# Optimization experiments

Measured on AMD Instinct MI355X. Metric: run time of the kernel, lower is better.

The kernel has to match this reference:

```python
import jax, jax.numpy as jnp
import numpy as np

D_QKV = 64

def setup_inputs() -> dict:
    key = jax.random.key(0)
    k1, k2, k3, k4 = jax.random.split(key, 4)
    B, T, D = 4, 2048, 1024
    x = jax.random.normal(k1, (B, T, D), dtype=jnp.float32)
    Wq = jax.random.normal(k2, (D, D_QKV), dtype=jnp.float32) * (D ** -0.5)
    Wk = jax.random.normal(k3, (D, D_QKV), dtype=jnp.float32) * (D ** -0.5)
    Wv = jax.random.normal(k4, (D, D_QKV), dtype=jnp.float32) * (D ** -0.5)
    return {"x": x, "Wq": Wq, "Wk": Wk, "Wv": Wv}

def reference(x, Wq, Wk, Wv):
    # x: [B, T, D]; single-head causal attention with head dim d_qkv
    T = x.shape[1]
    q = jnp.einsum("btd,de->bte", x, Wq)  # [B, T, d]
    k = jnp.einsum("btd,de->bte", x, Wk)
    v = jnp.einsum("btd,de->bte", x, Wv)
    scores = jnp.einsum("bqe,bke->bqk", q, k) / (D_QKV ** 0.5)  # [B, T, T]
    causal = jnp.tril(jnp.ones((T, T), dtype=bool))
    scores = jnp.where(causal, scores, -jnp.inf)
    attn = jax.nn.softmax(scores, axis=2)
    return jnp.einsum("bqk,bke->bqe", attn, v)  # [B, T, d]
```

## Files before the change

kernel.cpp:

```cpp
#include <hip/hip_runtime.h>
#include <hip/hip_bf16.h>

typedef __hip_bfloat16 bf16;
typedef __bf16 bf16x8 __attribute__((ext_vector_type(8)));
typedef float f32x4 __attribute__((ext_vector_type(4)));
typedef unsigned short u16x8 __attribute__((ext_vector_type(8)));

#define B_SZ   4
#define T_SEQ  2048
#define D_IN   1024
#define D_QKV  64
#define BT     (B_SZ * T_SEQ)
#define PSTR   72

#define GLD_LDS(gp, lp) __builtin_amdgcn_global_load_lds(                     \
    (const __attribute__((address_space(1))) void*)(gp),                      \
    (__attribute__((address_space(3))) void*)(lp), 16, 0, 0)

__global__ __launch_bounds__(256) void wt_prep(
    const float* __restrict__ Wq, const float* __restrict__ Wk,
    const float* __restrict__ Wv, bf16* __restrict__ wt)
{
    __shared__ float ws[64 * 65];
    const int bx = blockIdx.x;
    const int m  = bx >> 4;
    const int k0 = (bx & 15) << 6;
    const float* W = (m == 0) ? Wq : (m == 1) ? Wk : Wv;
    const int tid = threadIdx.x;
    #pragma unroll
    for (int i = 0; i < 16; ++i) {
        const int idx = i * 256 + tid;
        const int kk = idx >> 6, nn = idx & 63;
        ws[kk * 65 + nn] = W[(size_t)(k0 + kk) * D_QKV + nn];
    }
    __syncthreads();
    const int n = tid >> 2, kq = (tid & 3) << 4;
    bf16 tmp[16];
    #pragma unroll
    for (int j = 0; j < 16; ++j)
        tmp[j] = __float2bfloat16(ws[(kq + j) * 65 + n]);
    uint4* dst = (uint4*)(wt + (size_t)(m * 64 + n) * D_IN + k0 + kq);
    dst[0] = ((uint4*)tmp)[0];
    dst[1] = ((uint4*)tmp)[1];
}

__global__ __launch_bounds__(256) void qkv_proj_mfma(
    const float* __restrict__ x, const bf16* __restrict__ wt,
    bf16* __restrict__ qb, bf16* __restrict__ kb, bf16* __restrict__ vt)
{
    __shared__ uint4 As[2][512];
    __shared__ uint4 Bs[2][768];

    const int tid  = threadIdx.x;
    const int wave = tid >> 6;
    const int lane = tid & 63;
    const int col  = lane & 15;
    const int quad = lane >> 4;
    const int bx   = blockIdx.x;
    const int m0   = (bx >> 1) * 32;
    const int ng   = bx & 1;

    f32x4 acc[3];
    #pragma unroll
    for (int i = 0; i < 3; ++i) acc[i] = (f32x4){0.f, 0.f, 0.f, 0.f};

    auto stage = [&](int it, int buf) {
        const int k0 = it * 64;
        #pragma unroll
        for (int j = 0; j < 5; ++j) {
            const int s = wave + j * 4;
            if (s < 8) {
                const int c = s * 64 + lane;
                const int r = c >> 4;
                const int ccl = ((c & 15) - r) & 15;
                const float* g = x + (size_t)(m0 + r) * D_IN + k0 + ccl * 4;
                GLD_LDS(g, &As[buf][s * 64]);
            } else {
                const int bs = s - 8;
                const int c = bs * 64 + lane;
                const int n = c >> 3;
                const int ccl = ((c & 7) - n) & 7;
                const bf16* g = wt + (size_t)(ng * 96 + n) * D_IN + k0 + ccl * 8;
                GLD_LDS(g, &Bs[buf][bs * 64]);
            }
        }
    };

    stage(0, 0);
    const int r  = (wave >> 1) * 16 + col;
    const int nh = wave & 1;
    #pragma unroll 1
    for (int it = 0; it < 16; ++it) {
        __syncthreads();
        if (it + 1 < 16) stage(it + 1, (it + 1) & 1);
        const float4* Ac = (const float4*)As[it & 1];
        const uint4*  Bc = Bs[it & 1];
        #pragma unroll
        for (int s = 0; s < 2; ++s) {
            const int ca = s * 8 + quad * 2;
            const float4 a0 = Ac[r * 16 + ((ca + r) & 15)];
            const float4 a1 = Ac[r * 16 + ((ca + 1 + r) & 15)];
            const bf16x8 af = (bf16x8){(__bf16)a0.x, (__bf16)a0.y, (__bf16)a0.z, (__bf16)a0.w,
                                       (__bf16)a1.x, (__bf16)a1.y, (__bf16)a1.z, (__bf16)a1.w};
            #pragma unroll
            for (int i = 0; i < 3; ++i) {
                const int n = nh * 48 + i * 16 + col;
                const bf16x8 bfr = __builtin_bit_cast(bf16x8,
                    Bc[n * 8 + ((s * 4 + quad + n) & 7)]);
                acc[i] = __builtin_amdgcn_mfma_f32_16x16x32_bf16(af, bfr, acc[i], 0, 0, 0);
            }
        }
    }

    const int bb = m0 >> 11;
    const int tl = m0 & (T_SEQ - 1);
    #pragma unroll
    for (int i = 0; i < 3; ++i) {
        const int n = ng * 96 + nh * 48 + i * 16 + col;
        #pragma unroll
        for (int rr = 0; rr < 4; ++rr) {
            const int row = m0 + (wave >> 1) * 16 + quad * 4 + rr;
            const bf16 vq = __float2bfloat16(acc[i][rr]);
            if (n < 64)       qb[(size_t)row * D_QKV + n] = vq;
            else if (n < 128) kb[(size_t)row * D_QKV + (n - 64)] = vq;
            else              vt[(size_t)bb * D_QKV * T_SEQ + (size_t)(n - 128) * T_SEQ
                                 + (tl + (wave >> 1) * 16 + quad * 4 + rr)] = vq;
        }
    }
}

__global__ __launch_bounds__(256) void attn_kernel(
    const bf16* __restrict__ qb, const bf16* __restrict__ kb,
    const bf16* __restrict__ vt, float* __restrict__ Op, float* __restrict__ lp)
{
    __shared__ uint4 Ks[2][512];
    __shared__ uint4 Vs[2][512];
    __shared__ unsigned short plds[4 * 16 * PSTR];

    const int tid  = threadIdx.x;
    const int wave = tid >> 6;
    const int lane = tid & 63;
    const int col  = lane & 15;
    const int quad = lane >> 4;
    const int bx   = blockIdx.x;
    const int tile    = (bx < 256) ? (127 - (bx >> 2)) : ((bx - 256) >> 2);
    const int quarter = bx & 3;
    const int b    = tile >> 5;
    const int qloc = (tile & 31) * 64;
    const int nch  = (tile & 31) + 1;

    const bf16* kbp = kb + (size_t)b * T_SEQ * D_QKV;
    const bf16* vtp = vt + (size_t)b * D_QKV * T_SEQ;
    const uint4* q4 = (const uint4*)(qb + (size_t)b * T_SEQ * D_QKV);

    const bf16x8 aq0 = __builtin_bit_cast(bf16x8, q4[(qloc + wave * 16 + col) * 8 + quad]);
    const bf16x8 aq1 = __builtin_bit_cast(bf16x8, q4[(qloc + wave * 16 + col) * 8 + 4 + quad]);

    f32x4 o[4];
    float ls[4];
    #pragma unroll
    for (int dt = 0; dt < 4; ++dt) o[dt] = (f32x4){0.f, 0.f, 0.f, 0.f};
    #pragma unroll
    for (int rr = 0; rr < 4; ++rr) ls[rr] = 0.f;

    unsigned short* pl = plds + wave * 16 * PSTR;
    const u16x8* p8 = (const u16x8*)pl;

    auto stage = [&](int c, int buf) {
        const int kb0 = c * 64;
        #pragma unroll
        for (int j = 0; j < 4; ++j) {
            const int s = wave + j * 4;
            if (s < 8) {
                const int ch = s * 64 + lane;
                const int key = ch >> 3;
                const int ccl = ((ch & 7) - key) & 7;
                const bf16* g = kbp + (size_t)(kb0 + key) * D_QKV + ccl * 8;
                GLD_LDS(g, &Ks[buf][s * 64]);
            } else {
                const int vs = s - 8;
                const int ch = vs * 64 + lane;
                const int d = ch >> 3;
                const int ccl = ((ch & 7) - d) & 7;
                const bf16* g = vtp + (size_t)d * T_SEQ + kb0 + ccl * 8;
                GLD_LDS(g, &Vs[buf][vs * 64]);
            }
        }
    };

    if (quarter < nch) stage(quarter, 0);
    int i = 0;
    for (int c = quarter; c < nch; c += 4, ++i) {
        __syncthreads();
        if (c + 4 < nch) stage(c + 4, (i + 1) & 1);
        const uint4* Kc = Ks[i & 1];
        const uint4* Vc = Vs[i & 1];

        f32x4 sc[4];
        #pragma unroll
        for (int nt = 0; nt < 4; ++nt) {
            const int kp = nt * 16 + col;
            const bf16x8 bk0 = __builtin_bit_cast(bf16x8, Kc[kp * 8 + ((quad + kp) & 7)]);
            const bf16x8 bk1 = __builtin_bit_cast(bf16x8, Kc[kp * 8 + ((4 + quad + kp) & 7)]);
            sc[nt] = (f32x4){0.f, 0.f, 0.f, 0.f};
            sc[nt] = __builtin_amdgcn_mfma_f32_16x16x32_bf16(aq0, bk0, sc[nt], 0, 0, 0);
            sc[nt] = __builtin_amdgcn_mfma_f32_16x16x32_bf16(aq1, bk1, sc[nt], 0, 0, 0);
        }

        if (c == nch - 1) {
            #pragma unroll
            for (int nt = 0; nt < 4; ++nt) {
                const int kp = c * 64 + nt * 16 + col;
                #pragma unroll
                for (int rr = 0; rr < 4; ++rr)
                    if (kp > qloc + wave * 16 + quad * 4 + rr) sc[nt][rr] = -INFINITY;
            }
        }

        #pragma unroll
        for (int nt = 0; nt < 4; ++nt) {
            #pragma unroll
            for (int rr = 0; rr < 4; ++rr) {
                const float pv = __expf(sc[nt][rr] * 0.125f);
                ls[rr] += pv;
                pl[(quad * 4 + rr) * PSTR + nt * 16 + col] =
                    __builtin_bit_cast(unsigned short, __float2bfloat16(pv));
            }
        }

        const bf16x8 pa0 = __builtin_bit_cast(bf16x8, p8[col * 9 + quad]);
        const bf16x8 pa1 = __builtin_bit_cast(bf16x8, p8[col * 9 + 4 + quad]);

        #pragma unroll
        for (int dt = 0; dt < 4; ++dt) {
            const int dp = dt * 16 + col;
            const bf16x8 bv0 = __builtin_bit_cast(bf16x8, Vc[dp * 8 + ((quad + dp) & 7)]);
            const bf16x8 bv1 = __builtin_bit_cast(bf16x8, Vc[dp * 8 + ((4 + quad + dp) & 7)]);
            o[dt] = __builtin_amdgcn_mfma_f32_16x16x32_bf16(pa0, bv0, o[dt], 0, 0, 0);
            o[dt] = __builtin_amdgcn_mfma_f32_16x16x32_bf16(pa1, bv1, o[dt], 0, 0, 0);
        }
    }

    #pragma unroll
    for (int rr = 0; rr < 4; ++rr) {
        #pragma unroll
        for (int msk = 1; msk < 16; msk <<= 1)
            ls[rr] += __shfl_xor(ls[rr], msk);
    }

    const int pbase = (tile * 4 + quarter) * 64 + wave * 16;
    #pragma unroll
    for (int dt = 0; dt < 4; ++dt)
        #pragma unroll
        for (int rr = 0; rr < 4; ++rr)
            Op[(size_t)(pbase + quad * 4 + rr) * D_QKV + dt * 16 + col] = o[dt][rr];
    if (col == 0) {
        #pragma unroll
        for (int rr = 0; rr < 4; ++rr)
            lp[pbase + quad * 4 + rr] = ls[rr];
    }
}

__global__ __launch_bounds__(256) void combine_attn(
    const float* __restrict__ Op, const float* __restrict__ lp,
    float* __restrict__ out)
{
    const int idx = blockIdx.x * 256 + threadIdx.x;
    const int qg = idx >> 6, d = idx & 63;
    const int tile = qg >> 6, qq = qg & 63;
    float s = 0.f, l = 0.f;
    #pragma unroll
    for (int k = 0; k < 4; ++k) {
        s += Op[(size_t)((tile * 4 + k) * 64 + qq) * D_QKV + d];
        l += lp[(tile * 4 + k) * 64 + qq];
    }
    out[(size_t)qg * D_QKV + d] = s / l;
}

extern "C" void kernel_launch(void* const* d_in, const int* in_sizes, int n_in,
                              void* d_out, int out_size, void* d_ws, size_t ws_size,
                              hipStream_t stream) {
    const float* x  = (const float*)d_in[0];
    const float* Wq = (const float*)d_in[1];
    const float* Wk = (const float*)d_in[2];
    const float* Wv = (const float*)d_in[3];
    float* out = (float*)d_out;

    char* ws = (char*)d_ws;
    bf16*  qb = (bf16*)(ws);
    bf16*  kb = (bf16*)(ws + (1u << 20));
    bf16*  vt = (bf16*)(ws + (2u << 20));
    bf16*  wt = (bf16*)(ws + (3u << 20));
    float* Op = (float*)(ws + (4u << 20));
    float* lp = (float*)(ws + (12u << 20));

    wt_prep<<<48, 256, 0, stream>>>(Wq, Wk, Wv, wt);
    qkv_proj_mfma<<<512, 256, 0, stream>>>(x, wt, qb, kb, vt);
    attn_kernel<<<512, 256, 0, stream>>>(qb, kb, vt, Op, lp);
    combine_attn<<<2048, 256, 0, stream>>>(Op, lp, out);
}
```

Before: 109.5 us.

## Stream-K balance causal attention work and widen QKV projection tiles

The attention kernel now flattens all 2112 causal (query tile, key chunk) items and hands each of the 512 blocks an equal contiguous slice. A block carries its running accumulators across chunks of the same query tile and writes a partial result whenever a tile ends or its slice ends. The combine kernel walks each tile's chunks and sums only the partials written by distinct owning blocks. Separately, the QKV projection block now computes 16 rows against all 192 output columns, so x is read once instead of twice. The cost is a larger partial-output workspace (lp moved to 40MB) and a serial combine loop per query.

```diff
diff --git a/kernel.cpp b/kernel.cpp
--- a/kernel.cpp
+++ b/kernel.cpp
@@ -1,5 +1,6 @@
 #include <hip/hip_runtime.h>
 #include <hip/hip_bf16.h>
+#include <math.h>
 
 typedef __hip_bfloat16 bf16;
 typedef __bf16 bf16x8 __attribute__((ext_vector_type(8)));
@@ -12,6 +13,8 @@
 #define D_QKV  64
 #define BT     (B_SZ * T_SEQ)
 #define PSTR   72
+#define TOTW   2112
+#define ANB    512
 
 #define GLD_LDS(gp, lp) __builtin_amdgcn_global_load_lds(                     \
     (const __attribute__((address_space(1))) void*)(gp),                      \
@@ -48,17 +51,15 @@
     const float* __restrict__ x, const bf16* __restrict__ wt,
     bf16* __restrict__ qb, bf16* __restrict__ kb, bf16* __restrict__ vt)
 {
-    __shared__ uint4 As[2][512];
-    __shared__ uint4 Bs[2][768];
+    __shared__ uint4 As[2][256];
+    __shared__ uint4 Bs[2][1536];
 
     const int tid  = threadIdx.x;
     const int wave = tid >> 6;
     const int lane = tid & 63;
     const int col  = lane & 15;
     const int quad = lane >> 4;
-    const int bx   = blockIdx.x;
-    const int m0   = (bx >> 1) * 32;
-    const int ng   = bx & 1;
+    const int m0   = blockIdx.x * 16;
 
     f32x4 acc[3];
     #pragma unroll
@@ -67,28 +68,27 @@
     auto stage = [&](int it, int buf) {
         const int k0 = it * 64;
         #pragma unroll
-        for (int j = 0; j < 5; ++j) {
+        for (int j = 0; j < 7; ++j) {
             const int s = wave + j * 4;
-            if (s < 8) {
+            if (s < 4) {
                 const int c = s * 64 + lane;
                 const int r = c >> 4;
                 const int ccl = ((c & 15) - r) & 15;
                 const float* g = x + (size_t)(m0 + r) * D_IN + k0 + ccl * 4;
                 GLD_LDS(g, &As[buf][s * 64]);
             } else {
-                const int bs = s - 8;
+                const int bs = s - 4;
                 const int c = bs * 64 + lane;
                 const int n = c >> 3;
                 const int ccl = ((c & 7) - n) & 7;
-                const bf16* g = wt + (size_t)(ng * 96 + n) * D_IN + k0 + ccl * 8;
+                const bf16* g = wt + (size_t)n * D_IN + k0 + ccl * 8;
                 GLD_LDS(g, &Bs[buf][bs * 64]);
             }
         }
     };
 
     stage(0, 0);
-    const int r  = (wave >> 1) * 16 + col;
-    const int nh = wave & 1;
+    const int r = col;
     #pragma unroll 1
     for (int it = 0; it < 16; ++it) {
         __syncthreads();
@@ -104,7 +104,7 @@
                                        (__bf16)a1.x, (__bf16)a1.y, (__bf16)a1.z, (__bf16)a1.w};
             #pragma unroll
             for (int i = 0; i < 3; ++i) {
-                const int n = nh * 48 + i * 16 + col;
+                const int n = wave * 48 + i * 16 + col;
                 const bf16x8 bfr = __builtin_bit_cast(bf16x8,
                     Bc[n * 8 + ((s * 4 + quad + n) & 7)]);
                 acc[i] = __builtin_amdgcn_mfma_f32_16x16x32_bf16(af, bfr, acc[i], 0, 0, 0);
@@ -116,15 +116,15 @@
     const int tl = m0 & (T_SEQ - 1);
     #pragma unroll
     for (int i = 0; i < 3; ++i) {
-        const int n = ng * 96 + nh * 48 + i * 16 + col;
+        const int n = wave * 48 + i * 16 + col;
         #pragma unroll
         for (int rr = 0; rr < 4; ++rr) {
-            const int row = m0 + (wave >> 1) * 16 + quad * 4 + rr;
+            const int row = m0 + quad * 4 + rr;
             const bf16 vq = __float2bfloat16(acc[i][rr]);
             if (n < 64)       qb[(size_t)row * D_QKV + n] = vq;
             else if (n < 128) kb[(size_t)row * D_QKV + (n - 64)] = vq;
             else              vt[(size_t)bb * D_QKV * T_SEQ + (size_t)(n - 128) * T_SEQ
-                                 + (tl + (wave >> 1) * 16 + quad * 4 + rr)] = vq;
+                                 + (tl + quad * 4 + rr)] = vq;
         }
     }
 }
@@ -143,31 +143,25 @@
     const int col  = lane & 15;
     const int quad = lane >> 4;
     const int bx   = blockIdx.x;
-    const int tile    = (bx < 256) ? (127 - (bx >> 2)) : ((bx - 256) >> 2);
-    const int quarter = bx & 3;
-    const int b    = tile >> 5;
-    const int qloc = (tile & 31) * 64;
-    const int nch  = (tile & 31) + 1;
-
-    const bf16* kbp = kb + (size_t)b * T_SEQ * D_QKV;
-    const bf16* vtp = vt + (size_t)b * D_QKV * T_SEQ;
-    const uint4* q4 = (const uint4*)(qb + (size_t)b * T_SEQ * D_QKV);
-
-    const bf16x8 aq0 = __builtin_bit_cast(bf16x8, q4[(qloc + wave * 16 + col) * 8 + quad]);
-    const bf16x8 aq1 = __builtin_bit_cast(bf16x8, q4[(qloc + wave * 16 + col) * 8 + 4 + quad]);
-
-    f32x4 o[4];
-    float ls[4];
-    #pragma unroll
-    for (int dt = 0; dt < 4; ++dt) o[dt] = (f32x4){0.f, 0.f, 0.f, 0.f};
-    #pragma unroll
-    for (int rr = 0; rr < 4; ++rr) ls[rr] = 0.f;
+
+    const int lo = (bx * 33) >> 3;
+    const int hi = ((bx + 1) * 33) >> 3;
+    const int items = hi - lo;
+
+    int b = lo / 528;
+    int rres = lo - b * 528;
+    int t = (int)((sqrtf(8.f * (float)rres + 1.f) - 1.f) * 0.5f);
+    while ((t + 1) * (t + 2) / 2 <= rres) ++t;
+    while (t * (t + 1) / 2 > rres) --t;
+    int c = rres - t * (t + 1) / 2;
 
     unsigned short* pl = plds + wave * 16 * PSTR;
     const u16x8* p8 = (const u16x8*)pl;
 
-    auto stage = [&](int c, int buf) {
-        const int kb0 = c * 64;
+    auto stage = [&](int sb, int sc, int buf) {
+        const bf16* kbp = kb + (size_t)sb * T_SEQ * D_QKV;
+        const bf16* vtp = vt + (size_t)sb * D_QKV * T_SEQ;
+        const int kb0 = sc * 64;
         #pragma unroll
         for (int j = 0; j < 4; ++j) {
             const int s = wave + j * 4;
@@ -188,42 +182,63 @@
         }
     };
 
-    if (quarter < nch) stage(quarter, 0);
-    int i = 0;
-    for (int c = quarter; c < nch; c += 4, ++i) {
+    stage(b, c, 0);
+
+    bf16x8 aq0, aq1;
+    f32x4 o[4];
+    float ls[4];
+    int segw = lo;
+
+    #pragma unroll 1
+    for (int i = 0; i < items; ++i) {
+        if (i == 0 || c == 0) {
+            const uint4* q4 = (const uint4*)(qb + (size_t)b * T_SEQ * D_QKV);
+            const int qrow = t * 64 + wave * 16 + col;
+            aq0 = __builtin_bit_cast(bf16x8, q4[qrow * 8 + quad]);
+            aq1 = __builtin_bit_cast(bf16x8, q4[qrow * 8 + 4 + quad]);
+            #pragma unroll
+            for (int dt = 0; dt < 4; ++dt) o[dt] = (f32x4){0.f, 0.f, 0.f, 0.f};
+            #pragma unroll
+            for (int rr = 0; rr < 4; ++rr) ls[rr] = 0.f;
+            segw = lo + i;
+        }
+
+        int nb = b, nt = t, nc = c + 1;
+        if (nc > t) { nc = 0; ++nt; if (nt == 32) { nt = 0; ++nb; } }
+
         __syncthreads();
-        if (c + 4 < nch) stage(c + 4, (i + 1) & 1);
+        if (i + 1 < items) stage(nb, nc, (i + 1) & 1);
         const uint4* Kc = Ks[i & 1];
         const uint4* Vc = Vs[i & 1];
 
-        f32x4 sc[4];
-        #pragma unroll
-        for (int nt = 0; nt < 4; ++nt) {
-            const int kp = nt * 16 + col;
+        f32x4 sc4[4];
+        #pragma unroll
+        for (int nt2 = 0; nt2 < 4; ++nt2) {
+            const int kp = nt2 * 16 + col;
             const bf16x8 bk0 = __builtin_bit_cast(bf16x8, Kc[kp * 8 + ((quad + kp) & 7)]);
             const bf16x8 bk1 = __builtin_bit_cast(bf16x8, Kc[kp * 8 + ((4 + quad + kp) & 7)]);
-            sc[nt] = (f32x4){0.f, 0.f, 0.f, 0.f};
-            sc[nt] = __builtin_amdgcn_mfma_f32_16x16x32_bf16(aq0, bk0, sc[nt], 0, 0, 0);
-            sc[nt] = __builtin_amdgcn_mfma_f32_16x16x32_bf16(aq1, bk1, sc[nt], 0, 0, 0);
-        }
-
-        if (c == nch - 1) {
-            #pragma unroll
-            for (int nt = 0; nt < 4; ++nt) {
-                const int kp = c * 64 + nt * 16 + col;
+            sc4[nt2] = (f32x4){0.f, 0.f, 0.f, 0.f};
+            sc4[nt2] = __builtin_amdgcn_mfma_f32_16x16x32_bf16(aq0, bk0, sc4[nt2], 0, 0, 0);
+            sc4[nt2] = __builtin_amdgcn_mfma_f32_16x16x32_bf16(aq1, bk1, sc4[nt2], 0, 0, 0);
+        }
+
+        if (c == t) {
+            #pragma unroll
+            for (int nt2 = 0; nt2 < 4; ++nt2) {
+                const int kp = c * 64 + nt2 * 16 + col;
                 #pragma unroll
                 for (int rr = 0; rr < 4; ++rr)
-                    if (kp > qloc + wave * 16 + quad * 4 + rr) sc[nt][rr] = -INFINITY;
-            }
-        }
-
-        #pragma unroll
-        for (int nt = 0; nt < 4; ++nt) {
+                    if (kp > t * 64 + wave * 16 + quad * 4 + rr) sc4[nt2][rr] = -INFINITY;
+            }
+        }
+
+        #pragma unroll
+        for (int nt2 = 0; nt2 < 4; ++nt2) {
             #pragma unroll
             for (int rr = 0; rr < 4; ++rr) {
-                const float pv = __expf(sc[nt][rr] * 0.125f);
+                const float pv = __expf(sc4[nt2][rr] * 0.125f);
                 ls[rr] += pv;
-                pl[(quad * 4 + rr) * PSTR + nt * 16 + col] =
+                pl[(quad * 4 + rr) * PSTR + nt2 * 16 + col] =
                     __builtin_bit_cast(unsigned short, __float2bfloat16(pv));
             }
         }
@@ -239,25 +254,30 @@
             o[dt] = __builtin_amdgcn_mfma_f32_16x16x32_bf16(pa0, bv0, o[dt], 0, 0, 0);
             o[dt] = __builtin_amdgcn_mfma_f32_16x16x32_bf16(pa1, bv1, o[dt], 0, 0, 0);
         }
-    }
-
-    #pragma unroll
-    for (int rr = 0; rr < 4; ++rr) {
-        #pragma unroll
-        for (int msk = 1; msk < 16; msk <<= 1)
-            ls[rr] += __shfl_xor(ls[rr], msk);
-    }
-
-    const int pbase = (tile * 4 + quarter) * 64 + wave * 16;
-    #pragma unroll
-    for (int dt = 0; dt < 4; ++dt)
-        #pragma unroll
-        for (int rr = 0; rr < 4; ++rr)
-            Op[(size_t)(pbase + quad * 4 + rr) * D_QKV + dt * 16 + col] = o[dt][rr];
-    if (col == 0) {
-        #pragma unroll
-        for (int rr = 0; rr < 4; ++rr)
-            lp[pbase + quad * 4 + rr] = ls[rr];
+
+        if (c == t || i == items - 1) {
+            float lr[4];
+            #pragma unroll
+            for (int rr = 0; rr < 4; ++rr) {
+                lr[rr] = ls[rr];
+                #pragma unroll
+                for (int msk = 1; msk < 16; msk <<= 1)
+                    lr[rr] += __shfl_xor(lr[rr], msk);
+            }
+            const int pbase = segw * 64 + wave * 16;
+            #pragma unroll
+            for (int dt = 0; dt < 4; ++dt)
+                #pragma unroll
+                for (int rr = 0; rr < 4; ++rr)
+                    Op[(size_t)(pbase + quad * 4 + rr) * D_QKV + dt * 16 + col] = o[dt][rr];
+            if (col == 0) {
+                #pragma unroll
+                for (int rr = 0; rr < 4; ++rr)
+                    lp[pbase + quad * 4 + rr] = lr[rr];
+            }
+        }
+
+        b = nb; t = nt; c = nc;
     }
 }
 
@@ -267,12 +287,20 @@
 {
     const int idx = blockIdx.x * 256 + threadIdx.x;
     const int qg = idx >> 6, d = idx & 63;
-    const int tile = qg >> 6, qq = qg & 63;
+    const int g = qg >> 6, qq = qg & 63;
+    const int b = g >> 5, t = g & 31;
+    const int W0 = b * 528 + t * (t + 1) / 2;
     float s = 0.f, l = 0.f;
-    #pragma unroll
-    for (int k = 0; k < 4; ++k) {
-        s += Op[(size_t)((tile * 4 + k) * 64 + qq) * D_QKV + d];
-        l += lp[(tile * 4 + k) * 64 + qq];
+    int prevown = (8 * (W0 - 1) + 7) / 33;
+    #pragma unroll 1
+    for (int c = 0; c <= t; ++c) {
+        const int w = W0 + c;
+        const int own = (8 * w + 7) / 33;
+        if (c == 0 || own != prevown) {
+            s += Op[(size_t)(w * 64 + qq) * D_QKV + d];
+            l += lp[w * 64 + qq];
+        }
+        prevown = own;
     }
     out[(size_t)qg * D_QKV + d] = s / l;
 }
@@ -292,10 +320,10 @@
     bf16*  vt = (bf16*)(ws + (2u << 20));
     bf16*  wt = (bf16*)(ws + (3u << 20));
     float* Op = (float*)(ws + (4u << 20));
-    float* lp = (float*)(ws + (12u << 20));
+    float* lp = (float*)(ws + (40u << 20));
 
     wt_prep<<<48, 256, 0, stream>>>(Wq, Wk, Wv, wt);
     qkv_proj_mfma<<<512, 256, 0, stream>>>(x, wt, qb, kb, vt);
-    attn_kernel<<<512, 256, 0, stream>>>(qb, kb, vt, Op, lp);
+    attn_kernel<<<ANB, 256, 0, stream>>>(qb, kb, vt, Op, lp);
     combine_attn<<<2048, 256, 0, stream>>>(Op, lp, out);
 }
```

New measurement: 109.4 us, median of 2. Within noise of the previous version (-0.1%).
